# Kernel optimization log

Hardware: AMD Instinct MI355X
Metric: run time of the kernel (lower is better)

Reference implementation:

```python
import jax, jax.numpy as jnp
import numpy as np

B, D, C = 8192, 128, 64


def setup_inputs() -> dict:
    key = jax.random.key(0)
    k1, k2, k3 = jax.random.split(key, 3)
    embeddings = jax.random.normal(k1, (B, D), dtype=jnp.float32)
    margin_matrix = jax.random.uniform(k2, (C, C), dtype=jnp.float32)
    labels = jax.random.randint(k3, (B,), 0, C, dtype=jnp.int64)
    return {"embeddings": embeddings, "margin_matrix": margin_matrix, "labels": labels}


def reference(embeddings, margin_matrix, labels):
    # Batch-hard mining (indices only, mirrors the detached CPU loop).
    e = jax.lax.stop_gradient(embeddings)
    sq = jnp.sum(e * e, axis=1)                      # [B]
    d2 = sq[:, None] + sq[None, :] - 2.0 * (e @ e.T)  # [B, B] squared dists
    d2 = jnp.maximum(d2, 0.0)

    same = labels[:, None] == labels[None, :]         # [B, B]
    eye = jnp.eye(labels.shape[0], dtype=bool)
    pos_mask = same & ~eye
    neg_mask = ~same

    NEG_INF = jnp.float32(-1e30)
    POS_INF = jnp.float32(1e30)
    hard_pos = jnp.argmax(jnp.where(pos_mask, d2, NEG_INF), axis=1)  # hardest positive
    hard_neg = jnp.argmin(jnp.where(neg_mask, d2, POS_INF), axis=1)  # hardest negative
    valid = pos_mask.any(axis=1) & neg_mask.any(axis=1)

    # Recompute exact distances on differentiable embeddings (as torch.norm does).
    d_ap = jnp.linalg.norm(embeddings - embeddings[hard_pos], axis=1)
    d_an = jnp.linalg.norm(embeddings - embeddings[hard_neg], axis=1)
    margins = margin_matrix[labels, labels[hard_neg]]

    loss = jnp.maximum(d_ap - d_an + margins, 0.0)
    n_valid = jnp.sum(valid.astype(jnp.float32))
    return jnp.sum(jnp.where(valid, loss, 0.0)) / jnp.maximum(n_valid, 1.0)
```

## Files before the change

### kernel.cpp

```cpp
#include <hip/hip_runtime.h>

typedef __attribute__((ext_vector_type(8))) short bf16x8;
typedef __attribute__((ext_vector_type(4))) float f32x4;
typedef unsigned int u32;
typedef unsigned short u16;

#define BB 8192
#define DD 128
#define CC 64
#define NSLICE 16
#define SLICE_COLS 512
#define NTILES 8

typedef __attribute__((address_space(1))) void gvoid;
typedef __attribute__((address_space(3))) void lvoid;

static __device__ __forceinline__ u16 f2bf(float x) {
    u32 u = __float_as_uint(x);
    return (u16)((u + 0x7FFFu + ((u >> 16) & 1u)) >> 16);
}
static __device__ __forceinline__ u32 umaxu(u32 a, u32 b) { return a > b ? a : b; }
static __device__ __forceinline__ u32 uminu(u32 a, u32 b) { return a < b ? a : b; }

static __device__ __forceinline__ void gload16(const void* g, void* l) {
    __builtin_amdgcn_global_load_lds((const gvoid*)g, (lvoid*)l, 16, 0, 0);
}

__global__ __launch_bounds__(256) void k_prep(const float* __restrict__ E,
                                              float* __restrict__ sq,
                                              u16* __restrict__ Ebf) {
    int row = blockIdx.x * 4 + (threadIdx.x >> 6);
    int l   = threadIdx.x & 63;
    float2 v = *reinterpret_cast<const float2*>(E + (size_t)row * DD + l * 2);
    ushort2 bv = make_ushort2(f2bf(v.x), f2bf(v.y));
    *reinterpret_cast<ushort2*>(Ebf + (size_t)row * DD + l * 2) = bv;
    float s = v.x * v.x + v.y * v.y;
    #pragma unroll
    for (int m = 32; m; m >>= 1) s += __shfl_xor(s, m);
    if (l == 0) sq[row] = s;
}

__global__ __launch_bounds__(256, 2) void k_mine(const u16* __restrict__ Ebf,
                                                 const float* __restrict__ sq,
                                                 const int* __restrict__ lab,
                                                 u32* __restrict__ pmax,
                                                 u32* __restrict__ pmin) {
    __shared__ uint4 Bt4[2][1024];

    const int tid = threadIdx.x;
    const int l   = tid & 63;
    const int w   = tid >> 6;
    const int l15 = l & 15;
    const int l4  = l >> 4;
    const int rowW = blockIdx.x * 256 + w * 64;
    const int col0 = blockIdx.y * SLICE_COLS;

    bf16x8 a[4][4];
    #pragma unroll
    for (int rb = 0; rb < 4; ++rb)
        #pragma unroll
        for (int kk = 0; kk < 4; ++kk)
            a[rb][kk] = *reinterpret_cast<const bf16x8*>(
                Ebf + (size_t)(rowW + rb * 16 + l15) * DD + kk * 32 + l4 * 8);

    int labr[4][4];
    #pragma unroll
    for (int rb = 0; rb < 4; ++rb)
        #pragma unroll
        for (int e = 0; e < 4; ++e)
            labr[rb][e] = lab[rowW + rb * 16 + l4 * 4 + e];

    u32 kmax[4][4], kmin[4][4];
    #pragma unroll
    for (int rb = 0; rb < 4; ++rb)
        #pragma unroll
        for (int e = 0; e < 4; ++e) { kmax[rb][e] = 0u; kmin[rb][e] = 0xFFFFFFFFu; }

    const int srow = tid >> 4;
    const int sx   = (tid & 15) * 16;

    auto stage = [&](int bufi, int tt) {
        const char* gs = (const char*)Ebf + (size_t)(col0 + tt * 64) * 256;
        char* lb = (char*)&Bt4[bufi][0] + w * 1024;
        #pragma unroll
        for (int rd = 0; rd < 4; ++rd) {
            int r = rd * 16 + srow;
            gload16(gs + r * 256 + (sx ^ ((r & 7) << 4)), lb + rd * 4096);
        }
    };

    stage(0, 0);

    for (int t = 0; t < NTILES; ++t) {
        if (t + 1 < NTILES) {
            stage((t + 1) & 1, t + 1);
            asm volatile("s_waitcnt vmcnt(4)" ::: "memory");
        } else {
            asm volatile("s_waitcnt vmcnt(0)" ::: "memory");
        }
        __builtin_amdgcn_s_barrier();
        asm volatile("" ::: "memory");

        const char* Bt = (const char*)&Bt4[t & 1][0];
        const int colT = col0 + t * 64;

        float cbias[4]; int labc[4]; u32 jx[4], jn[4];
        #pragma unroll
        for (int cb = 0; cb < 4; ++cb) {
            int gj = colT + cb * 16 + l15;
            cbias[cb] = sq[gj] + 1024.0f;
            labc[cb]  = lab[gj];
            jn[cb] = (u32)gj;
            jx[cb] = (u32)(8191 - gj);
        }

        const bool isdiag = (rowW == colT);

        auto tilebody = [&](bool dg) {
            #pragma unroll
            for (int cb = 0; cb < 4; ++cb) {
                bf16x8 b[4];
                #pragma unroll
                for (int kk = 0; kk < 4; ++kk) {
                    int r = cb * 16 + l15;
                    b[kk] = *reinterpret_cast<const bf16x8*>(
                        Bt + r * 256 + ((kk * 64 + l4 * 16) ^ ((r & 7) << 4)));
                }
                f32x4 acc[4];
                #pragma unroll
                for (int rb = 0; rb < 4; ++rb) acc[rb] = (f32x4){0.f, 0.f, 0.f, 0.f};
                #pragma unroll
                for (int kk = 0; kk < 4; ++kk)
                    #pragma unroll
                    for (int rb = 0; rb < 4; ++rb)
                        acc[rb] = __builtin_amdgcn_mfma_f32_16x16x32_bf16(
                            a[rb][kk], b[kk], acc[rb], 0, 0, 0);

                #pragma unroll
                for (int rb = 0; rb < 4; ++rb)
                    #pragma unroll
                    for (int e = 0; e < 4; ++e) {
                        float val = fmaf(acc[rb][e], -2.0f, cbias[cb]);
                        u32 base = __float_as_uint(val) & 0xFFFFE000u;
                        bool eq = (labr[rb][e] == labc[cb]);
                        bool selfhit = dg && ((rb * 16 + l4 * 4 + e) == (cb * 16 + l15));
                        u32 cx = (eq && !selfhit) ? (base | jx[cb]) : 0u;
                        u32 cn = eq ? 0xFFFFFFFFu : (base | jn[cb]);
                        kmax[rb][e] = umaxu(kmax[rb][e], cx);
                        kmin[rb][e] = uminu(kmin[rb][e], cn);
                    }
            }
        };
        if (isdiag) tilebody(true); else tilebody(false);

        asm volatile("" ::: "memory");
        __builtin_amdgcn_s_barrier();
    }

    #pragma unroll
    for (int rb = 0; rb < 4; ++rb)
        #pragma unroll
        for (int e = 0; e < 4; ++e) {
            u32 kx = kmax[rb][e], kn = kmin[rb][e];
            #pragma unroll
            for (int m = 1; m < 16; m <<= 1) {
                u32 ox = (u32)__shfl_xor((int)kx, m); kx = umaxu(kx, ox);
                u32 on = (u32)__shfl_xor((int)kn, m); kn = uminu(kn, on);
            }
            if (l15 == 0) {
                int row = rowW + rb * 16 + l4 * 4 + e;
                pmax[(size_t)blockIdx.y * BB + row] = kx;
                pmin[(size_t)blockIdx.y * BB + row] = kn;
            }
        }
}

__global__ __launch_bounds__(256) void k_finalize(const float* __restrict__ E,
                                                  const float* __restrict__ M,
                                                  const int* __restrict__ lab,
                                                  const u32* __restrict__ pmax,
                                                  const u32* __restrict__ pmin,
                                                  float* __restrict__ loss,
                                                  float* __restrict__ validf) {
    int row = blockIdx.x * 4 + (threadIdx.x >> 6);
    int l   = threadIdx.x & 63;
    int l15 = l & 15;

    u32 kx = pmax[(size_t)l15 * BB + row];
    u32 kn = pmin[(size_t)l15 * BB + row];
    #pragma unroll
    for (int m = 1; m < 16; m <<= 1) {
        u32 ox = (u32)__shfl_xor((int)kx, m); kx = umaxu(kx, ox);
        u32 on = (u32)__shfl_xor((int)kn, m); kn = uminu(kn, on);
    }
    bool valid = (kx != 0u) && (kn != 0xFFFFFFFFu);
    int hp = 8191 - (int)(kx & 0x1FFFu);
    int hn = (int)(kn & 0x1FFFu);

    float2 ei = *reinterpret_cast<const float2*>(E + (size_t)row * DD + l * 2);
    float2 ep = *reinterpret_cast<const float2*>(E + (size_t)hp  * DD + l * 2);
    float2 en = *reinterpret_cast<const float2*>(E + (size_t)hn  * DD + l * 2);
    float dx = ei.x - ep.x, dy = ei.y - ep.y;
    float sap = dx * dx + dy * dy;
    dx = ei.x - en.x; dy = ei.y - en.y;
    float san = dx * dx + dy * dy;
    #pragma unroll
    for (int m = 32; m; m >>= 1) {
        sap += __shfl_xor(sap, m);
        san += __shfl_xor(san, m);
    }
    if (l == 0) {
        float dap = sqrtf(sap), dan = sqrtf(san);
        float mg = M[lab[row] * CC + lab[hn]];
        float lo = fmaxf(dap - dan + mg, 0.0f);
        loss[row]   = valid ? lo : 0.0f;
        validf[row] = valid ? 1.0f : 0.0f;
    }
}

__global__ __launch_bounds__(256) void k_reduce(const float* __restrict__ loss,
                                                const float* __restrict__ validf,
                                                float* __restrict__ out) {
    __shared__ float sl[256], sv[256];
    int tid = threadIdx.x;
    float a = 0.f, b = 0.f;
    for (int i = tid; i < BB; i += 256) { a += loss[i]; b += validf[i]; }
    sl[tid] = a; sv[tid] = b;
    __syncthreads();
    for (int s = 128; s; s >>= 1) {
        if (tid < s) { sl[tid] += sl[tid + s]; sv[tid] += sv[tid + s]; }
        __syncthreads();
    }
    if (tid == 0) out[0] = sl[0] / fmaxf(sv[0], 1.0f);
}

extern "C" void kernel_launch(void* const* d_in, const int* in_sizes, int n_in,
                              void* d_out, int out_size, void* d_ws, size_t ws_size,
                              hipStream_t stream) {
    const float* E   = (const float*)d_in[0];
    const float* M   = (const float*)d_in[1];
    const int*   lab = (const int*)d_in[2];
    float* out = (float*)d_out;

    char* ws = (char*)d_ws;
    u16*   Ebf  = (u16*)ws;        ws += (size_t)BB * DD * 2;
    float* sq   = (float*)ws;      ws += (size_t)BB * 4;
    u32*   pmax = (u32*)ws;        ws += (size_t)NSLICE * BB * 4;
    u32*   pmin = (u32*)ws;        ws += (size_t)NSLICE * BB * 4;
    float* loss = (float*)ws;      ws += (size_t)BB * 4;
    float* valf = (float*)ws;      ws += (size_t)BB * 4;

    k_prep<<<BB / 4, 256, 0, stream>>>(E, sq, Ebf);
    k_mine<<<dim3(BB / 256, NSLICE), 256, 0, stream>>>(Ebf, sq, lab, pmax, pmin);
    k_finalize<<<BB / 4, 256, 0, stream>>>(E, M, lab, pmax, pmin, loss, valf);
    k_reduce<<<1, 256, 0, stream>>>(loss, valf, out);
}
```

Baseline: 55.40 us.

## Triple-buffer LDS tiles to drop trailing barrier, use v_bfi for key packing

Moves the LDS staging from a double buffer to a rotating triple buffer, so the end-of-iteration barrier can be removed: the buffer written next is never the one being read this iteration. It also replaces the mask-and-OR key construction with a single v_bfi_b32 per key and precomputes the swizzled LDS read offsets outside the tile loop. The changes aim to cut one barrier per tile and some VALU work in the epilogue, at the cost of 16 KB more LDS per block, which could lower occupancy, and more registers held for the offsets.

```diff
diff --git a/kernel.cpp b/kernel.cpp
--- a/kernel.cpp
+++ b/kernel.cpp
@@ -21,6 +21,12 @@
 }
 static __device__ __forceinline__ u32 umaxu(u32 a, u32 b) { return a > b ? a : b; }
 static __device__ __forceinline__ u32 uminu(u32 a, u32 b) { return a < b ? a : b; }
+
+static __device__ __forceinline__ u32 bfi_key(u32 mask, u32 val, u32 idx) {
+    u32 r;
+    asm("v_bfi_b32 %0, %1, %2, %3" : "=v"(r) : "s"(mask), "v"(val), "v"(idx));
+    return r;
+}
 
 static __device__ __forceinline__ void gload16(const void* g, void* l) {
     __builtin_amdgcn_global_load_lds((const gvoid*)g, (lvoid*)l, 16, 0, 0);
@@ -45,7 +51,7 @@
                                                  const int* __restrict__ lab,
                                                  u32* __restrict__ pmax,
                                                  u32* __restrict__ pmin) {
-    __shared__ uint4 Bt4[2][1024];
+    __shared__ uint4 Bt4[3][1024];
 
     const int tid = threadIdx.x;
     const int l   = tid & 63;
@@ -76,6 +82,15 @@
         #pragma unroll
         for (int e = 0; e < 4; ++e) { kmax[rb][e] = 0u; kmin[rb][e] = 0xFFFFFFFFu; }
 
+    u32 boff[4][4];
+    #pragma unroll
+    for (int cb = 0; cb < 4; ++cb)
+        #pragma unroll
+        for (int kk = 0; kk < 4; ++kk) {
+            int r = cb * 16 + l15;
+            boff[cb][kk] = (u32)(r * 256 + ((kk * 64 + l4 * 16) ^ ((r & 7) << 4)));
+        }
+
     const int srow = tid >> 4;
     const int sx   = (tid & 15) * 16;
 
@@ -90,10 +105,13 @@
     };
 
     stage(0, 0);
+    const u32 HM = 0xFFFFE000u;
+    int cur = 0;
 
     for (int t = 0; t < NTILES; ++t) {
+        int nxt = cur + 1; if (nxt == 3) nxt = 0;
         if (t + 1 < NTILES) {
-            stage((t + 1) & 1, t + 1);
+            stage(nxt, t + 1);
             asm volatile("s_waitcnt vmcnt(4)" ::: "memory");
         } else {
             asm volatile("s_waitcnt vmcnt(0)" ::: "memory");
@@ -101,7 +119,7 @@
         __builtin_amdgcn_s_barrier();
         asm volatile("" ::: "memory");
 
-        const char* Bt = (const char*)&Bt4[t & 1][0];
+        const char* Bt = (const char*)&Bt4[cur][0];
         const int colT = col0 + t * 64;
 
         float cbias[4]; int labc[4]; u32 jx[4], jn[4];
@@ -110,8 +128,8 @@
             int gj = colT + cb * 16 + l15;
             cbias[cb] = sq[gj] + 1024.0f;
             labc[cb]  = lab[gj];
-            jn[cb] = (u32)gj;
-            jx[cb] = (u32)(8191 - gj);
+            jn[cb] = (u32)gj & 0x1FFFu;
+            jx[cb] = (u32)(8191 - gj) & 0x1FFFu;
         }
 
         const bool isdiag = (rowW == colT);
@@ -121,11 +139,8 @@
             for (int cb = 0; cb < 4; ++cb) {
                 bf16x8 b[4];
                 #pragma unroll
-                for (int kk = 0; kk < 4; ++kk) {
-                    int r = cb * 16 + l15;
-                    b[kk] = *reinterpret_cast<const bf16x8*>(
-                        Bt + r * 256 + ((kk * 64 + l4 * 16) ^ ((r & 7) << 4)));
-                }
+                for (int kk = 0; kk < 4; ++kk)
+                    b[kk] = *reinterpret_cast<const bf16x8*>(Bt + boff[cb][kk]);
                 f32x4 acc[4];
                 #pragma unroll
                 for (int rb = 0; rb < 4; ++rb) acc[rb] = (f32x4){0.f, 0.f, 0.f, 0.f};
@@ -141,11 +156,13 @@
                     #pragma unroll
                     for (int e = 0; e < 4; ++e) {
                         float val = fmaf(acc[rb][e], -2.0f, cbias[cb]);
-                        u32 base = __float_as_uint(val) & 0xFFFFE000u;
+                        u32 vb = __float_as_uint(val);
+                        u32 keyx = bfi_key(HM, vb, jx[cb]);
+                        u32 keyn = bfi_key(HM, vb, jn[cb]);
                         bool eq = (labr[rb][e] == labc[cb]);
                         bool selfhit = dg && ((rb * 16 + l4 * 4 + e) == (cb * 16 + l15));
-                        u32 cx = (eq && !selfhit) ? (base | jx[cb]) : 0u;
-                        u32 cn = eq ? 0xFFFFFFFFu : (base | jn[cb]);
+                        u32 cx = (eq && !selfhit) ? keyx : 0u;
+                        u32 cn = eq ? 0xFFFFFFFFu : keyn;
                         kmax[rb][e] = umaxu(kmax[rb][e], cx);
                         kmin[rb][e] = uminu(kmin[rb][e], cn);
                     }
@@ -153,8 +170,7 @@
         };
         if (isdiag) tilebody(true); else tilebody(false);
 
-        asm volatile("" ::: "memory");
-        __builtin_amdgcn_s_barrier();
+        cur = nxt;
     }
 
     #pragma unroll
```

Result: no change. 54.53 us (-1.6%).
